# Optimization experiments

Hardware: AMD Instinct MI355X
Metric: run time of the kernel (lower is better)

## Reference

```python
import jax, jax.numpy as jnp
import numpy as np
from jax import lax

B = 1024
LATENT = 512          # latent_dim (must equal conductor_output_dim, see forward feedback)
COND_H = 1024         # conductor_hidden_size
COND_OUT = 512        # conductor_output_dim
BOT_H = 1024          # bottom_decoder_hidden_size
OUT = 90              # output_size
NUM_SUB = 16          # hardcoded outer steps
SUB_LEN = 4           # hardcoded inner steps


def setup_inputs() -> dict:
    key = jax.random.key(0)
    ks = jax.random.split(key, 32)
    p = lambda k, shape: (jax.random.normal(k, shape, jnp.float32) * 0.02)
    bot_in = COND_OUT + OUT  # 602
    return {
        "z": jax.random.normal(ks[0], (B, LATENT), jnp.float32),
        "input_sequence": jax.random.uniform(ks[1], (B, NUM_SUB, SUB_LEN, OUT), jnp.float32),
        # fc_z
        "fc_z_w": p(ks[2], (COND_H, LATENT)), "fc_z_b": p(ks[3], (COND_H,)),
        # conductor LSTM (2 layers, torch gate order i,f,g,o)
        "cWih0": p(ks[4], (4 * COND_H, LATENT)), "cWhh0": p(ks[5], (4 * COND_H, COND_H)),
        "cbih0": p(ks[6], (4 * COND_H,)), "cbhh0": p(ks[7], (4 * COND_H,)),
        "cWih1": p(ks[8], (4 * COND_H, COND_H)), "cWhh1": p(ks[9], (4 * COND_H, COND_H)),
        "cbih1": p(ks[10], (4 * COND_H,)), "cbhh1": p(ks[11], (4 * COND_H,)),
        # fc_1 and conductor_fc
        "fc1_w": p(ks[12], (COND_OUT, COND_H)), "fc1_b": p(ks[13], (COND_OUT,)),
        "cfc_w": p(ks[14], (COND_OUT, COND_OUT)), "cfc_b": p(ks[15], (COND_OUT,)),
        # bottom decoder LSTM (2 layers)
        "bWih0": p(ks[16], (4 * BOT_H, bot_in)), "bWhh0": p(ks[17], (4 * BOT_H, BOT_H)),
        "bbih0": p(ks[18], (4 * BOT_H,)), "bbhh0": p(ks[19], (4 * BOT_H,)),
        "bWih1": p(ks[20], (4 * BOT_H, BOT_H)), "bWhh1": p(ks[21], (4 * BOT_H, BOT_H)),
        "bbih1": p(ks[22], (4 * BOT_H,)), "bbhh1": p(ks[23], (4 * BOT_H,)),
        # output layer
        "out_w": p(ks[24], (OUT, BOT_H)), "out_b": p(ks[25], (OUT,)),
    }


def _lstm_cell(x, h, c, Wih, Whh, bih, bhh):
    # torch LSTM cell: gates in i,f,g,o order
    gates = x @ Wih.T + bih + h @ Whh.T + bhh
    i, f, g, o = jnp.split(gates, 4, axis=-1)
    c_new = jax.nn.sigmoid(f) * c + jax.nn.sigmoid(i) * jnp.tanh(g)
    h_new = jax.nn.sigmoid(o) * jnp.tanh(c_new)
    return h_new, c_new


def reference(z, input_sequence, fc_z_w, fc_z_b,
              cWih0, cWhh0, cbih0, cbhh0, cWih1, cWhh1, cbih1, cbhh1,
              fc1_w, fc1_b, cfc_w, cfc_b,
              bWih0, bWhh0, bbih0, bbhh0, bWih1, bWhh1, bbih1, bbhh1,
              out_w, out_b):
    bsz = z.shape[0]
    out_dim = out_b.shape[0]
    bot_h = bWhh0.shape[1]

    # initial conductor state: tanh(fc_z(z)) used as (h, c) for both layers
    s0 = jnp.tanh(z @ fc_z_w.T + fc_z_b)  # [B, COND_H]
    cond_in0 = jnp.zeros((bsz, z.shape[1]), z.dtype)  # zeros(latent_dim)
    prev0 = jnp.zeros((bsz, out_dim), z.dtype)

    def outer(carry, _):
        cond_in, h1, c1, h2, c2, prev = carry
        h1, c1 = _lstm_cell(cond_in, h1, c1, cWih0, cWhh0, cbih0, cbhh0)
        h2, c2 = _lstm_cell(h1, h2, c2, cWih1, cWhh1, cbih1, cbhh1)
        cond_out = h2 @ fc1_w.T + fc1_b                    # [B, COND_OUT]
        emb = jnp.tanh(cond_out @ cfc_w.T + cfc_b)         # same every inner step
        z0 = jnp.zeros((bsz, bot_h), z.dtype)              # bottom state reset each subsequence

        def inner(ic, _):
            bh1, bc1, bh2, bc2, p = ic
            x = jnp.concatenate([emb, p], axis=1)          # [B, COND_OUT + OUT]
            bh1, bc1 = _lstm_cell(x, bh1, bc1, bWih0, bWhh0, bbih0, bbhh0)
            bh2, bc2 = _lstm_cell(bh1, bh2, bc2, bWih1, bWhh1, bbih1, bbhh1)
            p = bh2 @ out_w.T + out_b                      # [B, OUT]
            return (bh1, bc1, bh2, bc2, p), p

        (_, _, _, _, prev_last), ys = lax.scan(inner, (z0, z0, z0, z0, prev), None, length=SUB_LEN)
        # conductor_input for next step is fc_1 output (feedback in original code)
        return (cond_out, h1, c1, h2, c2, prev_last), ys   # ys: [SUB_LEN, B, OUT]

    _, outs = lax.scan(outer, (cond_in0, s0, s0, s0, s0, prev0), None, length=NUM_SUB)
    # outs: [NUM_SUB, SUB_LEN, B, OUT] -> [B, NUM_SUB*SUB_LEN, OUT]
    out = outs.reshape(NUM_SUB * SUB_LEN, bsz, out_dim).transpose(1, 0, 2)
    return jax.nn.sigmoid(out)
```

## Files before the change

### kernel.cpp

```cpp
#include <hip/hip_runtime.h>
#include <cstdint>
#include <cstddef>

typedef unsigned short u16;
typedef unsigned int u32;
typedef float f32x4 __attribute__((ext_vector_type(4)));
typedef _Float16 f16x8 __attribute__((ext_vector_type(8)));
typedef _Float16 f16x2 __attribute__((ext_vector_type(2)));

__device__ __forceinline__ u16 f2h(float x) {
  _Float16 h = (_Float16)x;
  return __builtin_bit_cast(u16, h);
}
__device__ __forceinline__ float sigm(float x) { return 1.f / (1.f + __expf(-x)); }

__device__ __forceinline__ void gll16(const void* g, void* l) {
  __builtin_amdgcn_global_load_lds(
      (const __attribute__((address_space(1))) void*)g,
      (__attribute__((address_space(3))) void*)l, 16, 0, 0);
}

__device__ __forceinline__ float dot8(f16x8 a, f16x8 b, float acc) {
  union U { f16x8 v; f16x2 h[4]; };
  U ua, ub;
  ua.v = a;
  ub.v = b;
#if __has_builtin(__builtin_amdgcn_fdot2)
#pragma unroll
  for (int i = 0; i < 4; ++i)
    acc = __builtin_amdgcn_fdot2(ua.h[i], ub.h[i], acc, false);
#else
#pragma unroll
  for (int i = 0; i < 8; ++i) acc += (float)a[i] * (float)b[i];
#endif
  return acc;
}

enum { M_PLAIN = 0, M_TANH = 1, M_FC2 = 3 };

struct GemmP {
  const u16* A; int lda;
  const u16* W; int ldw;
  int K;
  const float* bias;
  int mode;
  int czero;
  u16* d0; int ld0;
  u16* d1; int ld1;
  float* c0;
  float* c1;
};

template <bool CELL>
__global__ __launch_bounds__(512, 2) void gk(GemmP p) {
  __shared__ __align__(16) char sm[131072];
  const int tid = threadIdx.x;
  const int lane = tid & 63, wid = tid >> 6;
  const int wr = wid >> 1, wc = wid & 1;
  int bx, by;
  if (CELL) {
    const int hw = blockIdx.x;
    const int xcd = hw & 7, idx = hw >> 3;
    by = xcd * 4 + (idx >> 3);
    bx = idx & 7;
  } else {
    bx = blockIdx.x;
    by = blockIdx.y;
  }
  const int bRow = bx * 128;
  const int nBase = by * (CELL ? 32 : 128);
  const int col0 = lane & 15, g4 = lane >> 4;

  f32x4 acc[2][4];
#pragma unroll
  for (int m = 0; m < 2; ++m)
#pragma unroll
    for (int n = 0; n < 4; ++n) acc[m][n] = f32x4{0.f, 0.f, 0.f, 0.f};

  const char* Ab = (const char*)p.A;
  const char* Wb = (const char*)p.W;
  const size_t ldaB = (size_t)p.lda * 2, ldwB = (size_t)p.ldw * 2;

  auto stage = [&](int buf, int kt) {
    char* base = sm + buf * 32768;
    const int kb = kt * 128;
#pragma unroll
    for (int i = 0; i < 2; ++i) {
      const int s = i * 512 + tid;
      const int row = s >> 3, ch = s & 7;
      const int sch = ch ^ (row & 7);
      gll16(Ab + (size_t)(bRow + row) * ldaB + (size_t)(kb + sch * 16),
            base + s * 16);
      const int wrow = CELL ? ((row >> 5) * 1024 + nBase + (row & 31)) : (nBase + row);
      gll16(Wb + (size_t)wrow * ldwB + (size_t)(kb + sch * 16),
            base + 16384 + s * 16);
    }
  };

  const int nt = p.K >> 6;
  stage(0, 0);
  stage(1, 1);
  for (int t = 0; t < nt; ++t) {
    if (t + 2 < nt) stage((t + 2) & 3, t + 2);
    const int ahead = (nt - 1 - t < 2) ? (nt - 1 - t) : 2;
    if (ahead == 2)      asm volatile("s_waitcnt vmcnt(8)" ::: "memory");
    else if (ahead == 1) asm volatile("s_waitcnt vmcnt(4)" ::: "memory");
    else                 asm volatile("s_waitcnt vmcnt(0)" ::: "memory");
    __builtin_amdgcn_s_barrier();

    const char* Abase = sm + (t & 3) * 32768;
    const char* Wbase = Abase + 16384;
    f16x8 af[2][2], wf[2][4];
#pragma unroll
    for (int kf = 0; kf < 2; ++kf) {
      const int ch = kf * 4 + g4;
#pragma unroll
      for (int m = 0; m < 2; ++m) {
        const int r = wr * 32 + m * 16 + col0;
        af[kf][m] = *(const f16x8*)(Abase + r * 128 + ((ch ^ (r & 7)) << 4));
      }
#pragma unroll
      for (int n = 0; n < 4; ++n) {
        const int r = CELL ? (n * 32 + wc * 16 + col0) : (wc * 64 + n * 16 + col0);
        wf[kf][n] = *(const f16x8*)(Wbase + r * 128 + ((ch ^ (r & 7)) << 4));
      }
    }
#pragma unroll
    for (int kf = 0; kf < 2; ++kf)
#pragma unroll
      for (int m = 0; m < 2; ++m)
#pragma unroll
        for (int n = 0; n < 4; ++n)
          acc[m][n] = __builtin_amdgcn_mfma_f32_16x16x32_f16(af[kf][m], wf[kf][n],
                                                             acc[m][n], 0, 0, 0);
  }

  if (CELL) {
    const int j = nBase + wc * 16 + col0;
    const float bi = p.bias[j], bf_ = p.bias[j + 1024];
    const float bg = p.bias[j + 2048], bo = p.bias[j + 3072];
#pragma unroll
    for (int m = 0; m < 2; ++m) {
#pragma unroll
      for (int r = 0; r < 4; ++r) {
        const int b = bRow + wr * 32 + m * 16 + g4 * 4 + r;
        const float gi = acc[m][0][r] + bi;
        const float gf = acc[m][1][r] + bf_;
        const float gg = acc[m][2][r] + bg;
        const float go = acc[m][3][r] + bo;
        const size_t ci = (size_t)b * 1024 + j;
        const float cprev = p.czero ? 0.f : p.c0[ci];
        const float cn = sigm(gf) * cprev + sigm(gi) * tanhf(gg);
        p.c0[ci] = cn;
        const u16 hv = f2h(sigm(go) * tanhf(cn));
        p.d0[(size_t)b * p.ld0 + j] = hv;
        if (p.d1) p.d1[(size_t)b * p.ld1 + j] = hv;
      }
    }
  } else {
#pragma unroll
    for (int m = 0; m < 2; ++m)
#pragma unroll
      for (int n = 0; n < 4; ++n)
#pragma unroll
        for (int r = 0; r < 4; ++r) {
          const int b = bRow + wr * 32 + m * 16 + g4 * 4 + r;
          const int j = nBase + wc * 64 + n * 16 + col0;
          float v = acc[m][n][r] + p.bias[j];
          if (p.mode == M_TANH) {
            v = tanhf(v);
            const u16 hv = f2h(v);
            p.d0[(size_t)b * p.ld0 + j] = hv;
            if (p.d1) p.d1[(size_t)b * p.ld1 + j] = hv;
            if (p.c0) p.c0[(size_t)b * 1024 + j] = v;
            if (p.c1) p.c1[(size_t)b * 1024 + j] = v;
          } else if (p.mode == M_PLAIN) {
            p.d0[(size_t)b * p.ld0 + j] = f2h(v);
          } else {
            if (j < 512) p.d0[(size_t)b * p.ld0 + j] = f2h(v);
            else         p.d1[(size_t)b * p.ld1 + (j - 512)] = f2h(tanhf(v));
          }
        }
  }
}

__global__ __launch_bounds__(256, 4) void outk(const u16* A, const u16* W,
                                               const float* bias, u16* pdst,
                                               float* fout) {
  __shared__ __align__(16) u16 As[8][1024];
  const int tid = threadIdx.x;
  const int r0 = blockIdx.x * 8;
  const char* Ab = (const char*)A;
#pragma unroll
  for (int i = 0; i < 4; ++i) {
    const int s = i * 256 + tid;
    const int row = s >> 7, ch = s & 127;
    gll16(Ab + (size_t)(r0 + row) * 4096 + ch * 16, (char*)As + s * 16);
  }
  asm volatile("s_waitcnt vmcnt(0)" ::: "memory");
  __builtin_amdgcn_s_barrier();

  const int wid = tid >> 6, lane = tid & 63;
  const int c0 = lane * 2;
  if (c0 >= 90) return;
  const int row0 = wid * 2;
  const f16x8* a0 = (const f16x8*)As[row0];
  const f16x8* a1 = (const f16x8*)As[row0 + 1];
  const f16x8* w0 = (const f16x8*)(W + (size_t)c0 * 1024);
  const f16x8* w1 = (const f16x8*)(W + (size_t)(c0 + 1) * 1024);
  float acc00 = 0.f, acc01 = 0.f, acc10 = 0.f, acc11 = 0.f;
#pragma unroll 8
  for (int k = 0; k < 128; ++k) {
    const f16x8 wa = w0[k], wb = w1[k];
    const f16x8 aa = a0[k], ab = a1[k];
    acc00 = dot8(aa, wa, acc00);
    acc01 = dot8(aa, wb, acc01);
    acc10 = dot8(ab, wa, acc10);
    acc11 = dot8(ab, wb, acc11);
  }
  const float b0v = bias[c0], b1v = bias[c0 + 1];
  const int b0 = r0 + row0, b1 = b0 + 1;
  float v;
  v = acc00 + b0v;
  pdst[(size_t)b0 * 1664 + c0] = f2h(v);
  fout[(size_t)b0 * 5760 + c0] = sigm(v);
  v = acc01 + b1v;
  pdst[(size_t)b0 * 1664 + c0 + 1] = f2h(v);
  fout[(size_t)b0 * 5760 + c0 + 1] = sigm(v);
  v = acc10 + b0v;
  pdst[(size_t)b1 * 1664 + c0] = f2h(v);
  fout[(size_t)b1 * 5760 + c0] = sigm(v);
  v = acc11 + b1v;
  pdst[(size_t)b1 * 1664 + c0 + 1] = f2h(v);
  fout[(size_t)b1 * 5760 + c0 + 1] = sigm(v);
}


__global__ void pack_w(u16* dst, const float* a, int Ka, const float* b, int Kb,
                       int gap, int Kp, int srcRows) {
  const int r = blockIdx.y;
  const int c = blockIdx.x * 256 + threadIdx.x;
  if (c >= Kp) return;
  float v = 0.f;
  if (r < srcRows) {
    if (c < Ka) v = a[(size_t)r * Ka + c];
    else if (c >= Ka + gap && c < Ka + gap + Kb) v = b[(size_t)r * Kb + (c - Ka - gap)];
  }
  dst[(size_t)r * Kp + c] = f2h(v);
}

__global__ void pack_fc1T(u16* dst, const float* src) {
  const int idx = blockIdx.x * 256 + threadIdx.x;
  const int n = idx >> 9, j = idx & 511;
  dst[idx] = f2h(src[(size_t)j * 1024 + n]);
}

__global__ __launch_bounds__(256, 4) void bias_fused(float* bfc2, const float* cfc_w,
                                                     const float* fc1_b,
                                                     const float* cfc_b) {
  const int i = blockIdx.x * 4 + (threadIdx.x >> 6);
  const int lane = threadIdx.x & 63;
  const float4* wrow = (const float4*)(cfc_w + (size_t)i * 512);
  const float4* bv = (const float4*)fc1_b;
  float s = 0.f;
#pragma unroll
  for (int q = 0; q < 2; ++q) {
    const float4 a = wrow[lane * 2 + q], b = bv[lane * 2 + q];
    s += a.x * b.x + a.y * b.y + a.z * b.z + a.w * b.w;
  }
#pragma unroll
  for (int off = 32; off; off >>= 1) s += __shfl_xor(s, off);
  if (lane == 0) bfc2[512 + i] = s + cfc_b[i];
}

struct BiasAll {
  float *bz, *bc0, *bc1, *bfc2, *bb0, *bb1, *bout, *bzero;
  const float *fzb, *ci0, *ch0, *ci1, *ch1, *f1b, *bi0, *bh0, *bi1, *bh1, *ob;
};
__global__ void pack_biases(BiasAll q) {
  int i = blockIdx.x * 256 + threadIdx.x;
  if (i < 1024) { q.bz[i] = q.fzb[i]; return; } i -= 1024;
  if (i < 4096) { q.bc0[i] = q.ci0[i] + q.ch0[i]; return; } i -= 4096;
  if (i < 4096) { q.bc1[i] = q.ci1[i] + q.ch1[i]; return; } i -= 4096;
  if (i < 512)  { q.bfc2[i] = q.f1b[i]; return; } i -= 512;
  if (i < 4096) { q.bb0[i] = q.bi0[i] + q.bh0[i]; return; } i -= 4096;
  if (i < 4096) { q.bb1[i] = q.bi1[i] + q.bh1[i]; return; } i -= 4096;
  if (i < 128)  { q.bout[i] = (i < 90) ? q.ob[i] : 0.f; return; } i -= 128;
  if (i < 1024) { q.bzero[i] = 0.f; }
}

__global__ void conv_h(u16* dst, const float* src, long n) {
  for (long i = (long)blockIdx.x * blockDim.x + threadIdx.x; i < n;
       i += (long)gridDim.x * blockDim.x)
    dst[i] = f2h(src[i]);
}

__global__ void zero_init(u32* xc0, u32* xb0) {
  const int i = blockIdx.x * 256 + threadIdx.x;
  if (i < 1024 * 256) {
    xc0[(i >> 8) * 768 + (i & 255)] = 0;
  } else {
    const int k = i - 1024 * 256;
    xb0[(k >> 6) * 832 + 256 + (k & 63)] = 0;
  }
}

extern "C" void kernel_launch(void* const* d_in, const int* in_sizes, int n_in,
                              void* d_out, int out_size, void* d_ws, size_t ws_size,
                              hipStream_t stream) {
  const float* z      = (const float*)d_in[0];
  const float* fc_z_w = (const float*)d_in[2];
  const float* fc_z_b = (const float*)d_in[3];
  const float* cWih0  = (const float*)d_in[4];
  const float* cWhh0  = (const float*)d_in[5];
  const float* cbih0  = (const float*)d_in[6];
  const float* cbhh0  = (const float*)d_in[7];
  const float* cWih1  = (const float*)d_in[8];
  const float* cWhh1  = (const float*)d_in[9];
  const float* cbih1  = (const float*)d_in[10];
  const float* cbhh1  = (const float*)d_in[11];
  const float* fc1_w  = (const float*)d_in[12];
  const float* fc1_b  = (const float*)d_in[13];
  const float* cfc_w  = (const float*)d_in[14];
  const float* cfc_b  = (const float*)d_in[15];
  const float* bWih0  = (const float*)d_in[16];
  const float* bWhh0  = (const float*)d_in[17];
  const float* bbih0  = (const float*)d_in[18];
  const float* bbhh0  = (const float*)d_in[19];
  const float* bWih1  = (const float*)d_in[20];
  const float* bWhh1  = (const float*)d_in[21];
  const float* bbih1  = (const float*)d_in[22];
  const float* bbhh1  = (const float*)d_in[23];
  const float* out_w  = (const float*)d_in[24];
  const float* out_b  = (const float*)d_in[25];
  float* outp = (float*)d_out;

  char* w = (char*)d_ws;
  auto alloc = [&](size_t bytes) {
    char* p = w;
    w += (bytes + 255) & ~(size_t)255;
    return p;
  };
  u16* Wz    = (u16*)alloc((size_t)1024 * 512 * 2);
  u16* Wc0   = (u16*)alloc((size_t)4096 * 1536 * 2);
  u16* Wc1   = (u16*)alloc((size_t)4096 * 2048 * 2);
  u16* Wb0   = (u16*)alloc((size_t)4096 * 1664 * 2);
  u16* Wb1   = (u16*)alloc((size_t)4096 * 2048 * 2);
  u16* Wfc2  = (u16*)alloc((size_t)1024 * 1024 * 2);
  u16* Wcfc  = (u16*)alloc((size_t)512 * 512 * 2);
  u16* fc1T  = (u16*)alloc((size_t)1024 * 512 * 2);
  u16* Wout  = (u16*)alloc((size_t)128 * 1024 * 2);
  u16* zh    = (u16*)alloc((size_t)1024 * 512 * 2);
  u16* Xc0   = (u16*)alloc((size_t)1024 * 1536 * 2);
  u16* Xc1   = (u16*)alloc((size_t)1024 * 2048 * 2);
  u16* Xb0   = (u16*)alloc((size_t)1024 * 1664 * 2);
  u16* Xb1   = (u16*)alloc((size_t)1024 * 2048 * 2);
  float* cc0  = (float*)alloc((size_t)1024 * 1024 * 4);
  float* cc1  = (float*)alloc((size_t)1024 * 1024 * 4);
  float* cbb0 = (float*)alloc((size_t)1024 * 1024 * 4);
  float* cbb1 = (float*)alloc((size_t)1024 * 1024 * 4);
  float* bz   = (float*)alloc(1024 * 4);
  float* bc0  = (float*)alloc(4096 * 4);
  float* bc1  = (float*)alloc(4096 * 4);
  float* bfc2 = (float*)alloc(1024 * 4);
  float* bb0  = (float*)alloc(4096 * 4);
  float* bb1  = (float*)alloc(4096 * 4);
  float* bout = (float*)alloc(128 * 4);
  float* bzero= (float*)alloc(1024 * 4);

  const dim3 blk(256), blk5(512);
  const dim3 gcell(256);

  pack_w<<<dim3(2, 1024), blk, 0, stream>>>(Wz,   fc_z_w, 512,  nullptr, 0,    0,  512,  1024);
  pack_w<<<dim3(6, 4096), blk, 0, stream>>>(Wc0,  cWih0,  512,  cWhh0,   1024, 0,  1536, 4096);
  pack_w<<<dim3(8, 4096), blk, 0, stream>>>(Wc1,  cWih1,  1024, cWhh1,   1024, 0,  2048, 4096);
  pack_w<<<dim3(7, 4096), blk, 0, stream>>>(Wb0,  bWih0,  602,  bWhh0,   1024, 38, 1664, 4096);
  pack_w<<<dim3(8, 4096), blk, 0, stream>>>(Wb1,  bWih1,  1024, bWhh1,   1024, 0,  2048, 4096);
  pack_w<<<dim3(4, 512),  blk, 0, stream>>>(Wfc2, fc1_w,  1024, nullptr, 0,    0,  1024, 512);
  pack_w<<<dim3(2, 512),  blk, 0, stream>>>(Wcfc, cfc_w,  512,  nullptr, 0,    0,  512,  512);
  pack_w<<<dim3(4, 128),  blk, 0, stream>>>(Wout, out_w,  1024, nullptr, 0,    0,  1024, 90);
  pack_fc1T<<<dim3(2048), blk, 0, stream>>>(fc1T, fc1_w);
  {
    BiasAll q{bz, bc0, bc1, bfc2, bb0, bb1, bout, bzero,
              fc_z_b, cbih0, cbhh0, cbih1, cbhh1, fc1_b,
              bbih0, bbhh0, bbih1, bbhh1, out_b};
    pack_biases<<<dim3(80), blk, 0, stream>>>(q);
  }
  bias_fused<<<dim3(128), blk, 0, stream>>>(bfc2, cfc_w, fc1_b, cfc_b);
  conv_h<<<dim3(512), blk, 0, stream>>>(zh, z, 1024L * 512);
  zero_init<<<dim3(1280), blk, 0, stream>>>((u32*)Xc0, (u32*)Xb0);
  {
    GemmP p;
    p.A = Wcfc; p.lda = 512; p.W = fc1T; p.ldw = 512; p.K = 512; p.bias = bzero;
    p.mode = M_PLAIN; p.czero = 0;
    p.d0 = Wfc2 + (size_t)512 * 1024; p.ld0 = 1024; p.d1 = nullptr; p.ld1 = 0;
    p.c0 = nullptr; p.c1 = nullptr;
    gk<false><<<dim3(4, 8), blk5, 0, stream>>>(p);
  }

  {
    GemmP p;
    p.A = zh; p.lda = 512; p.W = Wz; p.ldw = 512; p.K = 512; p.bias = bz;
    p.mode = M_TANH; p.czero = 0;
    p.d0 = Xc0 + 512; p.ld0 = 1536; p.d1 = Xc1 + 1024; p.ld1 = 2048;
    p.c0 = cc0; p.c1 = cc1;
    gk<false><<<dim3(8, 8), blk5, 0, stream>>>(p);
  }

  for (int t = 0; t < 16; ++t) {
    {
      GemmP p;
      p.A = Xc0; p.lda = 1536; p.W = Wc0; p.ldw = 1536; p.K = 1536; p.bias = bc0;
      p.mode = 0; p.czero = 0;
      p.d0 = Xc0 + 512; p.ld0 = 1536; p.d1 = Xc1; p.ld1 = 2048;
      p.c0 = cc0; p.c1 = nullptr;
      gk<true><<<gcell, blk5, 0, stream>>>(p);
    }
    {
      GemmP p;
      p.A = Xc1; p.lda = 2048; p.W = Wc1; p.ldw = 2048; p.K = 2048; p.bias = bc1;
      p.mode = 0; p.czero = 0;
      p.d0 = Xc1 + 1024; p.ld0 = 2048; p.d1 = nullptr; p.ld1 = 0;
      p.c0 = cc1; p.c1 = nullptr;
      gk<true><<<gcell, blk5, 0, stream>>>(p);
    }
    {
      GemmP p;
      p.A = Xc1 + 1024; p.lda = 2048; p.W = Wfc2; p.ldw = 1024; p.K = 1024;
      p.bias = bfc2; p.mode = M_FC2; p.czero = 0;
      p.d0 = Xc0; p.ld0 = 1536; p.d1 = Xb0; p.ld1 = 1664;
      p.c0 = nullptr; p.c1 = nullptr;
      gk<false><<<dim3(8, 8), blk5, 0, stream>>>(p);
    }
    for (int s = 0; s < 4; ++s) {
      {
        GemmP p;
        p.A = Xb0; p.lda = 1664; p.W = Wb0; p.ldw = 1664;
        p.K = (s == 0) ? 640 : 1664; p.bias = bb0;
        p.mode = 0; p.czero = (s == 0);
        p.d0 = Xb0 + 640; p.ld0 = 1664; p.d1 = Xb1; p.ld1 = 2048;
        p.c0 = cbb0; p.c1 = nullptr;
        gk<true><<<gcell, blk5, 0, stream>>>(p);
      }
      {
        GemmP p;
        p.A = Xb1; p.lda = 2048; p.W = Wb1; p.ldw = 2048;
        p.K = (s == 0) ? 1024 : 2048; p.bias = bb1;
        p.mode = 0; p.czero = (s == 0);
        p.d0 = Xb1 + 1024; p.ld0 = 2048; p.d1 = nullptr; p.ld1 = 0;
        p.c0 = cbb1; p.c1 = nullptr;
        gk<true><<<gcell, blk5, 0, stream>>>(p);
      }
      outk<<<dim3(128), blk, 0, stream>>>(Xb1 + 1024, Wout, bout, Xb0 + 512,
                                          outp + (size_t)(t * 4 + s) * 90);
    }
  }
}
```

Before: 5.324 ms.

## Pre-pack LSTM weights into MFMA fragment order and load them directly to registers

Adds a pack_frag kernel that lays out the four LSTM gate weight matrices in per-block, per-wave MFMA fragment order. A new cell kernel loads these fragments straight from global memory into registers with double buffering, so only the activations go through LDS. This removes the weight LDS staging and halves LDS use per block, which may help occupancy and cut LDS traffic. The cost is that weight loads now depend on per-lane global latency with less overlap than the deeper LDS pipeline gave, plus a heavier one-time packing step.

```diff
diff --git a/kernel.cpp b/kernel.cpp
--- a/kernel.cpp
+++ b/kernel.cpp
@@ -7,6 +7,7 @@
 typedef float f32x4 __attribute__((ext_vector_type(4)));
 typedef _Float16 f16x8 __attribute__((ext_vector_type(8)));
 typedef _Float16 f16x2 __attribute__((ext_vector_type(2)));
+typedef unsigned short u16x8 __attribute__((ext_vector_type(8)));
 
 __device__ __forceinline__ u16 f2h(float x) {
   _Float16 h = (_Float16)x;
@@ -36,6 +37,128 @@
   return acc;
 }
 
+struct CellP {
+  const u16* A; int lda;
+  const u16* Wf;
+  int nt;
+  int ntFull;
+  const float* bias;
+  int czero;
+  u16* d0; int ld0;
+  u16* d1; int ld1;
+  float* c0;
+};
+
+__global__ __launch_bounds__(512, 2) void ck(CellP p) {
+  __shared__ __align__(16) char sm[65536];
+  const int tid = threadIdx.x;
+  const int lane = tid & 63, wid = tid >> 6;
+  const int wr = wid >> 1, wc = wid & 1;
+  const int hw = blockIdx.x;
+  const int xcd = hw & 7, idx = hw >> 3;
+  const int by = xcd * 4 + (idx >> 3);
+  const int bx = idx & 7;
+  const int bRow = bx * 128;
+  const int col0 = lane & 15, g4 = lane >> 4;
+  const int nt = p.nt;
+
+  f32x4 acc[2][4];
+#pragma unroll
+  for (int m = 0; m < 2; ++m)
+#pragma unroll
+    for (int n = 0; n < 4; ++n) acc[m][n] = f32x4{0.f, 0.f, 0.f, 0.f};
+
+  const char* Ab = (const char*)p.A;
+  const size_t ldaB = (size_t)p.lda * 2;
+
+  auto stageA = [&](int buf, int kt) {
+    char* base = sm + buf * 16384;
+    const int kb = kt * 128;
+#pragma unroll
+    for (int i = 0; i < 2; ++i) {
+      const int s = i * 512 + tid;
+      const int row = s >> 3, ch = s & 7;
+      const int sch = ch ^ (row & 7);
+      gll16(Ab + (size_t)(bRow + row) * ldaB + (size_t)(kb + sch * 16),
+            base + s * 16);
+    }
+  };
+
+  const char* Wfb = (const char*)p.Wf +
+                    ((size_t)(by * p.ntFull) * 2 + wc) * 8192 + lane * 16;
+  auto loadW = [&](f16x8 (&wf)[2][4], int kt) {
+    const char* b = Wfb + (size_t)kt * 16384;
+#pragma unroll
+    for (int kf = 0; kf < 2; ++kf)
+#pragma unroll
+      for (int n = 0; n < 4; ++n)
+        wf[kf][n] = *(const f16x8*)(b + (kf * 4 + n) * 1024);
+  };
+
+  auto step = [&](int u, const f16x8 (&wf)[2][4]) {
+    const bool w1 = (u + 1 < nt), w2 = (u + 2 < nt);
+    if (w1 && w2) asm volatile("s_waitcnt vmcnt(12)" ::: "memory");
+    else if (w1)  asm volatile("s_waitcnt vmcnt(10)" ::: "memory");
+    else          asm volatile("s_waitcnt vmcnt(0)" ::: "memory");
+    __builtin_amdgcn_s_barrier();
+    const char* Abase = sm + (u & 3) * 16384;
+    f16x8 af[2][2];
+#pragma unroll
+    for (int kf = 0; kf < 2; ++kf) {
+      const int ch = kf * 4 + g4;
+#pragma unroll
+      for (int m = 0; m < 2; ++m) {
+        const int r = wr * 32 + m * 16 + col0;
+        af[kf][m] = *(const f16x8*)(Abase + r * 128 + ((ch ^ (r & 7)) << 4));
+      }
+    }
+#pragma unroll
+    for (int kf = 0; kf < 2; ++kf)
+#pragma unroll
+      for (int m = 0; m < 2; ++m)
+#pragma unroll
+        for (int n = 0; n < 4; ++n)
+          acc[m][n] = __builtin_amdgcn_mfma_f32_16x16x32_f16(af[kf][m], wf[kf][n],
+                                                             acc[m][n], 0, 0, 0);
+  };
+
+  f16x8 wfA[2][4], wfB[2][4];
+  stageA(0, 0);
+  stageA(1, 1);
+  loadW(wfA, 0);
+  for (int t = 0; t < nt; t += 2) {
+    if (t + 1 < nt) loadW(wfB, t + 1);
+    if (t + 2 < nt) stageA((t + 2) & 3, t + 2);
+    step(t, wfA);
+    if (t + 1 >= nt) break;
+    if (t + 2 < nt) loadW(wfA, t + 2);
+    if (t + 3 < nt) stageA((t + 3) & 3, t + 3);
+    step(t + 1, wfB);
+  }
+
+  const int j = by * 32 + wc * 16 + col0;
+  const float bi = p.bias[j], bf_ = p.bias[j + 1024];
+  const float bg = p.bias[j + 2048], bo = p.bias[j + 3072];
+#pragma unroll
+  for (int m = 0; m < 2; ++m) {
+#pragma unroll
+    for (int r = 0; r < 4; ++r) {
+      const int b = bRow + wr * 32 + m * 16 + g4 * 4 + r;
+      const float gi = acc[m][0][r] + bi;
+      const float gf = acc[m][1][r] + bf_;
+      const float gg = acc[m][2][r] + bg;
+      const float go = acc[m][3][r] + bo;
+      const size_t ci = (size_t)b * 1024 + j;
+      const float cprev = p.czero ? 0.f : p.c0[ci];
+      const float cn = sigm(gf) * cprev + sigm(gi) * tanhf(gg);
+      p.c0[ci] = cn;
+      const u16 hv = f2h(sigm(go) * tanhf(cn));
+      p.d0[(size_t)b * p.ld0 + j] = hv;
+      if (p.d1) p.d1[(size_t)b * p.ld1 + j] = hv;
+    }
+  }
+}
+
 enum { M_PLAIN = 0, M_TANH = 1, M_FC2 = 3 };
 
 struct GemmP {
@@ -44,31 +167,19 @@
   int K;
   const float* bias;
   int mode;
-  int czero;
   u16* d0; int ld0;
   u16* d1; int ld1;
   float* c0;
   float* c1;
 };
 
-template <bool CELL>
 __global__ __launch_bounds__(512, 2) void gk(GemmP p) {
   __shared__ __align__(16) char sm[131072];
   const int tid = threadIdx.x;
   const int lane = tid & 63, wid = tid >> 6;
   const int wr = wid >> 1, wc = wid & 1;
-  int bx, by;
-  if (CELL) {
-    const int hw = blockIdx.x;
-    const int xcd = hw & 7, idx = hw >> 3;
-    by = xcd * 4 + (idx >> 3);
-    bx = idx & 7;
-  } else {
-    bx = blockIdx.x;
-    by = blockIdx.y;
-  }
-  const int bRow = bx * 128;
-  const int nBase = by * (CELL ? 32 : 128);
+  const int bRow = blockIdx.x * 128;
+  const int nBase = blockIdx.y * 128;
   const int col0 = lane & 15, g4 = lane >> 4;
 
   f32x4 acc[2][4];
@@ -91,8 +202,7 @@
       const int sch = ch ^ (row & 7);
       gll16(Ab + (size_t)(bRow + row) * ldaB + (size_t)(kb + sch * 16),
             base + s * 16);
-      const int wrow = CELL ? ((row >> 5) * 1024 + nBase + (row & 31)) : (nBase + row);
-      gll16(Wb + (size_t)wrow * ldwB + (size_t)(kb + sch * 16),
+      gll16(Wb + (size_t)(nBase + row) * ldwB + (size_t)(kb + sch * 16),
             base + 16384 + s * 16);
     }
   };
@@ -121,7 +231,7 @@
       }
 #pragma unroll
       for (int n = 0; n < 4; ++n) {
-        const int r = CELL ? (n * 32 + wc * 16 + col0) : (wc * 64 + n * 16 + col0);
+        const int r = wc * 64 + n * 16 + col0;
         wf[kf][n] = *(const f16x8*)(Wbase + r * 128 + ((ch ^ (r & 7)) << 4));
       }
     }
@@ -135,53 +245,29 @@
                                                              acc[m][n], 0, 0, 0);
   }
 
-  if (CELL) {
-    const int j = nBase + wc * 16 + col0;
-    const float bi = p.bias[j], bf_ = p.bias[j + 1024];
-    const float bg = p.bias[j + 2048], bo = p.bias[j + 3072];
-#pragma unroll
-    for (int m = 0; m < 2; ++m) {
+#pragma unroll
+  for (int m = 0; m < 2; ++m)
+#pragma unroll
+    for (int n = 0; n < 4; ++n)
 #pragma unroll
       for (int r = 0; r < 4; ++r) {
         const int b = bRow + wr * 32 + m * 16 + g4 * 4 + r;
-        const float gi = acc[m][0][r] + bi;
-        const float gf = acc[m][1][r] + bf_;
-        const float gg = acc[m][2][r] + bg;
-        const float go = acc[m][3][r] + bo;
-        const size_t ci = (size_t)b * 1024 + j;
-        const float cprev = p.czero ? 0.f : p.c0[ci];
-        const float cn = sigm(gf) * cprev + sigm(gi) * tanhf(gg);
-        p.c0[ci] = cn;
-        const u16 hv = f2h(sigm(go) * tanhf(cn));
-        p.d0[(size_t)b * p.ld0 + j] = hv;
-        if (p.d1) p.d1[(size_t)b * p.ld1 + j] = hv;
+        const int j = nBase + wc * 64 + n * 16 + col0;
+        float v = acc[m][n][r] + p.bias[j];
+        if (p.mode == M_TANH) {
+          v = tanhf(v);
+          const u16 hv = f2h(v);
+          p.d0[(size_t)b * p.ld0 + j] = hv;
+          if (p.d1) p.d1[(size_t)b * p.ld1 + j] = hv;
+          if (p.c0) p.c0[(size_t)b * 1024 + j] = v;
+          if (p.c1) p.c1[(size_t)b * 1024 + j] = v;
+        } else if (p.mode == M_PLAIN) {
+          p.d0[(size_t)b * p.ld0 + j] = f2h(v);
+        } else {
+          if (j < 512) p.d0[(size_t)b * p.ld0 + j] = f2h(v);
+          else         p.d1[(size_t)b * p.ld1 + (j - 512)] = f2h(tanhf(v));
+        }
       }
-    }
-  } else {
-#pragma unroll
-    for (int m = 0; m < 2; ++m)
-#pragma unroll
-      for (int n = 0; n < 4; ++n)
-#pragma unroll
-        for (int r = 0; r < 4; ++r) {
-          const int b = bRow + wr * 32 + m * 16 + g4 * 4 + r;
-          const int j = nBase + wc * 64 + n * 16 + col0;
-          float v = acc[m][n][r] + p.bias[j];
-          if (p.mode == M_TANH) {
-            v = tanhf(v);
-            const u16 hv = f2h(v);
-            p.d0[(size_t)b * p.ld0 + j] = hv;
-            if (p.d1) p.d1[(size_t)b * p.ld1 + j] = hv;
-            if (p.c0) p.c0[(size_t)b * 1024 + j] = v;
-            if (p.c1) p.c1[(size_t)b * 1024 + j] = v;
-          } else if (p.mode == M_PLAIN) {
-            p.d0[(size_t)b * p.ld0 + j] = f2h(v);
-          } else {
-            if (j < 512) p.d0[(size_t)b * p.ld0 + j] = f2h(v);
-            else         p.d1[(size_t)b * p.ld1 + (j - 512)] = f2h(tanhf(v));
-          }
-        }
-  }
 }
 
 __global__ __launch_bounds__(256, 4) void outk(const u16* A, const u16* W,
@@ -235,6 +321,40 @@
   fout[(size_t)b1 * 5760 + c0 + 1] = sigm(v);
 }
 
+
+struct FragP {
+  u16* dst;
+  const float* a; int Ka, sa;
+  const float* b; int Kb, sb;
+  int gap;
+  int nt;
+};
+__global__ void pack_frag(FragP f) {
+  const long ci = (long)blockIdx.x * 256 + threadIdx.x;
+  const long total = (long)512 * (f.nt * 64);
+  if (ci >= total) return;
+  const int lane = (int)(ci & 63);
+  const int n = (int)((ci >> 6) & 3);
+  const int kf = (int)((ci >> 8) & 1);
+  const int wc = (int)((ci >> 9) & 1);
+  const long r2 = ci >> 10;
+  const int t = (int)(r2 % f.nt);
+  const int by = (int)(r2 / f.nt);
+  const int r = n * 32 + wc * 16 + (lane & 15);
+  const int g = (r >> 5) * 1024 + by * 32 + (r & 31);
+  const int k0 = t * 64 + (kf * 4 + (lane >> 4)) * 8;
+  u16x8 out;
+#pragma unroll
+  for (int e = 0; e < 8; ++e) {
+    const int k = k0 + e;
+    float v = 0.f;
+    if (k < f.Ka) v = f.a[(size_t)g * f.sa + k];
+    else if (k >= f.Ka + f.gap && k < f.Ka + f.gap + f.Kb)
+      v = f.b[(size_t)g * f.sb + (k - f.Ka - f.gap)];
+    out[e] = f2h(v);
+  }
+  *(u16x8*)(f.dst + ci * 8) = out;
+}
 
 __global__ void pack_w(u16* dst, const float* a, int Ka, const float* b, int Kb,
                        int gap, int Kp, int srcRows) {
@@ -341,11 +461,11 @@
     w += (bytes + 255) & ~(size_t)255;
     return p;
   };
+  u16* Wc0f  = (u16*)alloc((size_t)4096 * 1536 * 2);
+  u16* Wc1f  = (u16*)alloc((size_t)4096 * 2048 * 2);
+  u16* Wb0f  = (u16*)alloc((size_t)4096 * 1664 * 2);
+  u16* Wb1f  = (u16*)alloc((size_t)4096 * 2048 * 2);
   u16* Wz    = (u16*)alloc((size_t)1024 * 512 * 2);
-  u16* Wc0   = (u16*)alloc((size_t)4096 * 1536 * 2);
-  u16* Wc1   = (u16*)alloc((size_t)4096 * 2048 * 2);
-  u16* Wb0   = (u16*)alloc((size_t)4096 * 1664 * 2);
-  u16* Wb1   = (u16*)alloc((size_t)4096 * 2048 * 2);
   u16* Wfc2  = (u16*)alloc((size_t)1024 * 1024 * 2);
   u16* Wcfc  = (u16*)alloc((size_t)512 * 512 * 2);
   u16* fc1T  = (u16*)alloc((size_t)1024 * 512 * 2);
@@ -371,14 +491,26 @@
   const dim3 blk(256), blk5(512);
   const dim3 gcell(256);
 
-  pack_w<<<dim3(2, 1024), blk, 0, stream>>>(Wz,   fc_z_w, 512,  nullptr, 0,    0,  512,  1024);
-  pack_w<<<dim3(6, 4096), blk, 0, stream>>>(Wc0,  cWih0,  512,  cWhh0,   1024, 0,  1536, 4096);
-  pack_w<<<dim3(8, 4096), blk, 0, stream>>>(Wc1,  cWih1,  1024, cWhh1,   1024, 0,  2048, 4096);
-  pack_w<<<dim3(7, 4096), blk, 0, stream>>>(Wb0,  bWih0,  602,  bWhh0,   1024, 38, 1664, 4096);
-  pack_w<<<dim3(8, 4096), blk, 0, stream>>>(Wb1,  bWih1,  1024, bWhh1,   1024, 0,  2048, 4096);
-  pack_w<<<dim3(4, 512),  blk, 0, stream>>>(Wfc2, fc1_w,  1024, nullptr, 0,    0,  1024, 512);
-  pack_w<<<dim3(2, 512),  blk, 0, stream>>>(Wcfc, cfc_w,  512,  nullptr, 0,    0,  512,  512);
-  pack_w<<<dim3(4, 128),  blk, 0, stream>>>(Wout, out_w,  1024, nullptr, 0,    0,  1024, 90);
+  {
+    FragP f{Wc0f, cWih0, 512, 512, cWhh0, 1024, 1024, 0, 24};
+    pack_frag<<<dim3(3072), blk, 0, stream>>>(f);
+  }
+  {
+    FragP f{Wc1f, cWih1, 1024, 1024, cWhh1, 1024, 1024, 0, 32};
+    pack_frag<<<dim3(4096), blk, 0, stream>>>(f);
+  }
+  {
+    FragP f{Wb0f, bWih0, 602, 602, bWhh0, 1024, 1024, 38, 26};
+    pack_frag<<<dim3(3328), blk, 0, stream>>>(f);
+  }
+  {
+    FragP f{Wb1f, bWih1, 1024, 1024, bWhh1, 1024, 1024, 0, 32};
+    pack_frag<<<dim3(4096), blk, 0, stream>>>(f);
+  }
+  pack_w<<<dim3(2, 1024), blk, 0, stream>>>(Wz,   fc_z_w, 512,  nullptr, 0, 0, 512,  1024);
+  pack_w<<<dim3(4, 512),  blk, 0, stream>>>(Wfc2, fc1_w,  1024, nullptr, 0, 0, 1024, 512);
+  pack_w<<<dim3(2, 512),  blk, 0, stream>>>(Wcfc, cfc_w,  512,  nullptr, 0, 0, 512,  512);
+  pack_w<<<dim3(4, 128),  blk, 0, stream>>>(Wout, out_w,  1024, nullptr, 0, 0, 1024, 90);
   pack_fc1T<<<dim3(2048), blk, 0, stream>>>(fc1T, fc1_w);
   {
     BiasAll q{bz, bc0, bc1, bfc2, bb0, bb1, bout, bzero,
@@ -390,66 +522,42 @@
   conv_h<<<dim3(512), blk, 0, stream>>>(zh, z, 1024L * 512);
   zero_init<<<dim3(1280), blk, 0, stream>>>((u32*)Xc0, (u32*)Xb0);
   {
-    GemmP p;
-    p.A = Wcfc; p.lda = 512; p.W = fc1T; p.ldw = 512; p.K = 512; p.bias = bzero;
-    p.mode = M_PLAIN; p.czero = 0;
-    p.d0 = Wfc2 + (size_t)512 * 1024; p.ld0 = 1024; p.d1 = nullptr; p.ld1 = 0;
-    p.c0 = nullptr; p.c1 = nullptr;
-    gk<false><<<dim3(4, 8), blk5, 0, stream>>>(p);
-  }
-
-  {
-    GemmP p;
-    p.A = zh; p.lda = 512; p.W = Wz; p.ldw = 512; p.K = 512; p.bias = bz;
-    p.mode = M_TANH; p.czero = 0;
-    p.d0 = Xc0 + 512; p.ld0 = 1536; p.d1 = Xc1 + 1024; p.ld1 = 2048;
-    p.c0 = cc0; p.c1 = cc1;
-    gk<false><<<dim3(8, 8), blk5, 0, stream>>>(p);
+    GemmP p{Wcfc, 512, fc1T, 512, 512, bzero, M_PLAIN,
+            Wfc2 + (size_t)512 * 1024, 1024, nullptr, 0, nullptr, nullptr};
+    gk<<<dim3(4, 8), blk5, 0, stream>>>(p);
+  }
+  {
+    GemmP p{zh, 512, Wz, 512, 512, bz, M_TANH,
+            Xc0 + 512, 1536, Xc1 + 1024, 2048, cc0, cc1};
+    gk<<<dim3(8, 8), blk5, 0, stream>>>(p);
   }
 
   for (int t = 0; t < 16; ++t) {
     {
-      GemmP p;
-      p.A = Xc0; p.lda = 1536; p.W = Wc0; p.ldw = 1536; p.K = 1536; p.bias = bc0;
-      p.mode = 0; p.czero = 0;
-      p.d0 = Xc0 + 512; p.ld0 = 1536; p.d1 = Xc1; p.ld1 = 2048;
-      p.c0 = cc0; p.c1 = nullptr;
-      gk<true><<<gcell, blk5, 0, stream>>>(p);
+      CellP p{Xc0, 1536, Wc0f, 24, 24, bc0, 0,
+              Xc0 + 512, 1536, Xc1, 2048, cc0};
+      ck<<<gcell, blk5, 0, stream>>>(p);
     }
     {
-      GemmP p;
-      p.A = Xc1; p.lda = 2048; p.W = Wc1; p.ldw = 2048; p.K = 2048; p.bias = bc1;
-      p.mode = 0; p.czero = 0;
-      p.d0 = Xc1 + 1024; p.ld0 = 2048; p.d1 = nullptr; p.ld1 = 0;
-      p.c0 = cc1; p.c1 = nullptr;
-      gk<true><<<gcell, blk5, 0, stream>>>(p);
+      CellP p{Xc1, 2048, Wc1f, 32, 32, bc1, 0,
+              Xc1 + 1024, 2048, nullptr, 0, cc1};
+      ck<<<gcell, blk5, 0, stream>>>(p);
     }
     {
-      GemmP p;
-      p.A = Xc1 + 1024; p.lda = 2048; p.W = Wfc2; p.ldw = 1024; p.K = 1024;
-      p.bias = bfc2; p.mode = M_FC2; p.czero = 0;
-      p.d0 = Xc0; p.ld0 = 1536; p.d1 = Xb0; p.ld1 = 1664;
-      p.c0 = nullptr; p.c1 = nullptr;
-      gk<false><<<dim3(8, 8), blk5, 0, stream>>>(p);
+      GemmP p{Xc1 + 1024, 2048, Wfc2, 1024, 1024, bfc2, M_FC2,
+              Xc0, 1536, Xb0, 1664, nullptr, nullptr};
+      gk<<<dim3(8, 8), blk5, 0, stream>>>(p);
     }
     for (int s = 0; s < 4; ++s) {
       {
-        GemmP p;
-        p.A = Xb0; p.lda = 1664; p.W = Wb0; p.ldw = 1664;
-        p.K = (s == 0) ? 640 : 1664; p.bias = bb0;
-        p.mode = 0; p.czero = (s == 0);
-        p.d0 = Xb0 + 640; p.ld0 = 1664; p.d1 = Xb1; p.ld1 = 2048;
-        p.c0 = cbb0; p.c1 = nullptr;
-        gk<true><<<gcell, blk5, 0, stream>>>(p);
+        CellP p{Xb0, 1664, Wb0f, (s == 0) ? 10 : 26, 26, bb0, (s == 0),
+                Xb0 + 640, 1664, Xb1, 2048, cbb0};
+        ck<<<gcell, blk5, 0, stream>>>(p);
       }
       {
-        GemmP p;
-        p.A = Xb1; p.lda = 2048; p.W = Wb1; p.ldw = 2048;
-        p.K = (s == 0) ? 1024 : 2048; p.bias = bb1;
-        p.mode = 0; p.czero = (s == 0);
-        p.d0 = Xb1 + 1024; p.ld0 = 2048; p.d1 = nullptr; p.ld1 = 0;
-        p.c0 = cbb1; p.c1 = nullptr;
-        gk<true><<<gcell, blk5, 0, stream>>>(p);
+        CellP p{Xb1, 2048, Wb1f, (s == 0) ? 16 : 32, 32, bb1, (s == 0),
+                Xb1 + 1024, 2048, nullptr, 0, cbb1};
+        ck<<<gcell, blk5, 0, stream>>>(p);
       }
       outk<<<dim3(128), blk, 0, stream>>>(Xb1 + 1024, Wout, bout, Xb0 + 512,
                                           outp + (size_t)(t * 4 + s) * 90);
```

Measured after the change: 6.116 ms. +14.9%, slower.
